# Optimization experiments

Measured on AMD Instinct MI355X. Metric: run time of the kernel, lower is better.

## Reference

```python
import jax, jax.numpy as jnp
import numpy as np

EPS = 1e-5          # nn.LayerNorm default eps
THRESH = 0.4        # min_entity_score
K = 20              # max_entities_per_text
NUM_TYPES = 8       # len(EntityType) (not in source; fixed constant)


def _mlp(x, w1, b1, g, be, w2, b2):
    """Linear -> LayerNorm -> GELU(exact) -> (Dropout=eval identity) -> Linear."""
    h = x @ w1 + b1
    mu = h.mean(-1, keepdims=True)
    var = ((h - mu) ** 2).mean(-1, keepdims=True)
    h = (h - mu) * jax.lax.rsqrt(var + EPS) * g + be
    h = jax.nn.gelu(h, approximate=False)
    return h @ w2 + b2


def setup_inputs() -> dict:
    key = jax.random.key(0)
    ks = jax.random.split(key, 10)
    B, S, D, H, T = 8, 4096, 1024, 256, NUM_TYPES

    def lin(k, i, o):
        s = 1.0 / np.sqrt(i)
        return jax.random.uniform(k, (i, o), jnp.float32, -s, s)

    return {
        "hidden_states": jax.random.normal(ks[0], (B, S, D), jnp.float32),
        "attention_mask": jax.random.randint(ks[1], (B, S), 0, 2).astype(jnp.int32),
        # entity_scorer params
        "sc_w1": lin(ks[2], D, H), "sc_b1": jnp.zeros((H,), jnp.float32),
        "sc_g": jnp.ones((H,), jnp.float32), "sc_be": jnp.zeros((H,), jnp.float32),
        "sc_w2": lin(ks[3], H, 1), "sc_b2": jnp.zeros((1,), jnp.float32),
        # span_enhancer params
        "en_w1": lin(ks[4], D, H), "en_b1": jnp.zeros((H,), jnp.float32),
        "en_g": jnp.ones((H,), jnp.float32), "en_be": jnp.zeros((H,), jnp.float32),
        "en_w2": lin(ks[5], H, D), "en_b2": jnp.zeros((D,), jnp.float32),
        # type_classifier params
        "ty_w1": lin(ks[6], D, H), "ty_b1": jnp.zeros((H,), jnp.float32),
        "ty_g": jnp.ones((H,), jnp.float32), "ty_be": jnp.zeros((H,), jnp.float32),
        "ty_w2": lin(ks[7], H, T), "ty_b2": jnp.zeros((T,), jnp.float32),
    }


def reference(hidden_states, attention_mask,
              sc_w1, sc_b1, sc_g, sc_be, sc_w2, sc_b2,
              en_w1, en_b1, en_g, en_be, en_w2, en_b2,
              ty_w1, ty_b1, ty_g, ty_be, ty_w2, ty_b2):
    B, S, D = hidden_states.shape
    # per-token entity scores [B, S]
    scores = jax.nn.sigmoid(_mlp(hidden_states, sc_w1, sc_b1, sc_g, sc_be, sc_w2, sc_b2))[..., 0]
    scores = scores * attention_mask.astype(scores.dtype)
    # parallel run-length encoding of spans (replaces serial python loop):
    # a token is inside a span iff score >= thresh and unmasked; spans break on
    # below-threshold or masked tokens, exactly as the serial RLE does.
    above = (scores >= THRESH) & (attention_mask > 0)
    prev = jnp.pad(above[:, :-1], ((0, 0), (1, 0)))
    start = above & ~prev
    sid = jnp.clip(jnp.cumsum(start.astype(jnp.int32), axis=1) - 1, 0)  # span label per token
    seg = (sid + jnp.arange(B, dtype=jnp.int32)[:, None] * S).reshape(-1)
    w = above.astype(scores.dtype)
    nseg = B * S
    span_len = jax.ops.segment_sum(w.reshape(-1), seg, num_segments=nseg).reshape(B, S)
    span_sum = jax.ops.segment_sum((scores * w).reshape(-1), seg, num_segments=nseg).reshape(B, S)
    rep_sum = jax.ops.segment_sum((hidden_states * w[..., None]).reshape(B * S, D), seg,
                                  num_segments=nseg).reshape(B, S, D)
    denom = jnp.maximum(span_len, 1.0)
    avg = span_sum / denom                      # mean token score per span
    valid = (span_len > 0) & (avg >= THRESH)    # avg-score threshold from original
    sel = jnp.where(valid, avg, -1.0)
    # keep at most K highest-scoring spans per batch row (matches global sort + per-batch cap)
    top_vals, top_idx = jax.lax.top_k(sel, K)   # [B, K]
    valid_k = (top_vals >= THRESH).astype(scores.dtype)
    reps = jnp.take_along_axis(rep_sum, top_idx[..., None], axis=1)
    lens = jnp.take_along_axis(denom, top_idx, axis=1)
    reps = reps / lens[..., None] * valid_k[..., None]      # span mean-pooled hidden states
    enhanced = _mlp(reps, en_w1, en_b1, en_g, en_be, en_w2, en_b2) * valid_k[..., None]
    type_logits = _mlp(enhanced, ty_w1, ty_b1, ty_g, ty_be, ty_w2, ty_b2)
    type_probs = jax.nn.softmax(type_logits, axis=-1)
    entity_types = jnp.argmax(type_logits, axis=-1)
    entity_scores = top_vals * valid_k
    return scores, enhanced, type_logits, entity_scores, type_probs, entity_types, valid_k
```

## Files before the change

kernel.cpp:

```cpp
#include <hip/hip_runtime.h>
#include <hip/hip_bf16.h>

#define S_LEN 4096
#define BATCH 8
#define DMODEL 1024
#define HDIM 256
#define NTYPES 8
#define KMAX 20
#define NSLOT (BATCH*KMAX)
#define THRESH 0.4f
#define LN_EPS 1e-5f
#define RSQRT2 0.70710678118654752f

#define O_SCORES 0
#define O_ENH    32768
#define O_TLOG   196608
#define O_ESC    197888
#define O_TPROB  198048
#define O_TYPE   199328
#define O_VALIDK 199488

#define WS_SCORES   0
#define WS_SPSTART  32768
#define WS_SPLEN    49152
#define WS_SPAVG    65536
#define WS_NSP      81920
#define WS_SELSTART 81936
#define WS_SELLEN   82096
#define WS_SELAVG   82256
#define WS_SELVALID 82416
#define WS_IMG      82576

typedef _Float16 f16x2 __attribute__((ext_vector_type(2)));
typedef _Float16 f16x8 __attribute__((ext_vector_type(8)));
typedef float f32x16 __attribute__((ext_vector_type(16)));

__device__ __forceinline__ float gelu_exact(float v) {
    return 0.5f * v * (1.0f + erff(v * RSQRT2));
}

__global__ __launch_bounds__(256) void k_prep(
    const float* __restrict__ W1, _Float16* __restrict__ IMG)
{
    const int c = blockIdx.x;
    const int n = threadIdx.x;
    f16x8 hv[2], lv[2];
#pragma unroll
    for (int j = 0; j < 2; j++)
#pragma unroll
        for (int e = 0; e < 8; e++) {
            float w = W1[(size_t)(c * 16 + j * 8 + e) * HDIM + n];
            _Float16 h = (_Float16)w;
            hv[j][e] = h;
            lv[j][e] = (_Float16)(w - (float)h);
        }
    const int off = c * 8192 + n * 16;
    *(f16x8*)&IMG[off] = hv[0];
    *(f16x8*)&IMG[off + 8] = hv[1];
    *(f16x8*)&IMG[off + 4096] = lv[0];
    *(f16x8*)&IMG[off + 4096 + 8] = lv[1];
}

__global__ __launch_bounds__(512, 4) void k_score6(
    const float* __restrict__ X, const _Float16* __restrict__ IMG,
    const float* __restrict__ B1, const float* __restrict__ G,
    const float* __restrict__ BE, const float* __restrict__ W2,
    const float* __restrict__ B2, const int* __restrict__ MASK,
    float* __restrict__ scf, float* __restrict__ out)
{
    union SM {
        _Float16 A[2][2][1024];
        struct { float part2[64 * 5]; float mul[64]; float rsl[64]; } e;
    };
    __shared__ SM sm;

    const int tid = threadIdx.x;
    const int lane = tid & 63, wid = tid >> 6;
    const int lr = lane & 31, lh = lane >> 5;
    const int wm = (wid & 1) * 32;
    const int wn = (wid >> 1) * 64;
    const int wnid = wid >> 1;
    const int tok0 = blockIdx.x * 64;

    const int xrow = tid >> 3, xk = (tid & 7) * 2;
    const float* xbase = X + (size_t)(tok0 + xrow) * DMODEL + xk;
    const int awoff = xrow * 16 + xk;
    const int aroff = (wm + lr) * 16 + lh * 8;
    const int bo0 = (wn + lr) * 16 + lh * 8;
    const int bo1 = (wn + 32 + lr) * 16 + lh * 8;

    f32x16 acc0 = (f32x16)0.0f, acc1 = (f32x16)0.0f;

    float2 x0 = *(const float2*)xbase;
    f16x8 bh0c = *(const f16x8*)&IMG[bo0];
    f16x8 bh1c = *(const f16x8*)&IMG[bo1];
    f16x8 bl0c = *(const f16x8*)&IMG[4096 + bo0];
    f16x8 bl1c = *(const f16x8*)&IMG[4096 + bo1];
    {
        _Float16 h0 = (_Float16)x0.x, h1 = (_Float16)x0.y;
        f16x2 hh = {h0, h1};
        f16x2 ll = {(_Float16)(x0.x - (float)h0), (_Float16)(x0.y - (float)h1)};
        *(f16x2*)&sm.A[0][0][awoff] = hh;
        *(f16x2*)&sm.A[0][1][awoff] = ll;
    }
    float2 xnext = *(const float2*)(xbase + 16);
    f16x8 bh0n = *(const f16x8*)&IMG[8192 + bo0];
    f16x8 bh1n = *(const f16x8*)&IMG[8192 + bo1];
    f16x8 bl0n = *(const f16x8*)&IMG[8192 + 4096 + bo0];
    f16x8 bl1n = *(const f16x8*)&IMG[8192 + 4096 + bo1];
    asm volatile("s_waitcnt lgkmcnt(0)" ::: "memory");
    __builtin_amdgcn_s_barrier();
    __builtin_amdgcn_sched_barrier(0);

    int cur = 0;
#pragma unroll 2
    for (int c = 0; c < 64; ++c) {
        const int cf = (c + 2) & 63;
        float2 xfut = *(const float2*)(xbase + cf * 16);
        const _Float16* ib = IMG + cf * 8192;
        f16x8 fbh0 = *(const f16x8*)&ib[bo0];
        f16x8 fbh1 = *(const f16x8*)&ib[bo1];
        f16x8 fbl0 = *(const f16x8*)&ib[4096 + bo0];
        f16x8 fbl1 = *(const f16x8*)&ib[4096 + bo1];

        f16x8 fah = *(const f16x8*)&sm.A[cur][0][aroff];
        f16x8 fal = *(const f16x8*)&sm.A[cur][1][aroff];

        acc0 = __builtin_amdgcn_mfma_f32_32x32x16_f16(fah, bh0c, acc0, 0, 0, 0);
        acc0 = __builtin_amdgcn_mfma_f32_32x32x16_f16(fal, bh0c, acc0, 0, 0, 0);
        acc0 = __builtin_amdgcn_mfma_f32_32x32x16_f16(fah, bl0c, acc0, 0, 0, 0);
        acc1 = __builtin_amdgcn_mfma_f32_32x32x16_f16(fah, bh1c, acc1, 0, 0, 0);
        acc1 = __builtin_amdgcn_mfma_f32_32x32x16_f16(fal, bh1c, acc1, 0, 0, 0);
        acc1 = __builtin_amdgcn_mfma_f32_32x32x16_f16(fah, bl1c, acc1, 0, 0, 0);

        {
            _Float16 h0 = (_Float16)xnext.x, h1 = (_Float16)xnext.y;
            f16x2 hh = {h0, h1};
            f16x2 ll = {(_Float16)(xnext.x - (float)h0), (_Float16)(xnext.y - (float)h1)};
            *(f16x2*)&sm.A[cur ^ 1][0][awoff] = hh;
            *(f16x2*)&sm.A[cur ^ 1][1][awoff] = ll;
        }
        asm volatile("s_waitcnt lgkmcnt(0)" ::: "memory");
        __builtin_amdgcn_s_barrier();
        __builtin_amdgcn_sched_barrier(0);

        bh0c = bh0n; bh1c = bh1n; bl0c = bl0n; bl1c = bl1n;
        bh0n = fbh0; bh1n = fbh1; bl0n = fbl0; bl1n = fbl1;
        xnext = xfut;
        cur ^= 1;
    }

    __syncthreads();

    float bcol[2], gcol[2], becol[2], wcol[2];
#pragma unroll
    for (int ni = 0; ni < 2; ni++) {
        int colg = wn + ni * 32 + lr;
        bcol[ni] = B1[colg];
        gcol[ni] = G[colg];
        becol[ni] = BE[colg];
        wcol[ni] = W2[colg];
    }
#pragma unroll
    for (int r = 0; r < 16; r++) { acc0[r] += bcol[0]; acc1[r] += bcol[1]; }

#pragma unroll
    for (int r = 0; r < 16; r++) {
        float p = acc0[r] + acc1[r];
        p += __shfl_xor(p, 1);  p += __shfl_xor(p, 2);
        p += __shfl_xor(p, 4);  p += __shfl_xor(p, 8);
        p += __shfl_xor(p, 16);
        int row = wm + (r & 3) + 8 * (r >> 2) + 4 * lh;
        if (lr == 0) sm.e.part2[row * 5 + wnid] = p;
    }
    __syncthreads();
    if (tid < 64)
        sm.e.mul[tid] = (sm.e.part2[tid * 5] + sm.e.part2[tid * 5 + 1] +
                         sm.e.part2[tid * 5 + 2] + sm.e.part2[tid * 5 + 3]) * (1.0f / 256.0f);
    __syncthreads();
#pragma unroll
    for (int r = 0; r < 16; r++) {
        int row = wm + (r & 3) + 8 * (r >> 2) + 4 * lh;
        float m = sm.e.mul[row];
        float d0 = acc0[r] - m, d1 = acc1[r] - m;
        float p = d0 * d0 + d1 * d1;
        p += __shfl_xor(p, 1);  p += __shfl_xor(p, 2);
        p += __shfl_xor(p, 4);  p += __shfl_xor(p, 8);
        p += __shfl_xor(p, 16);
        if (lr == 0) sm.e.part2[row * 5 + wnid] = p;
    }
    __syncthreads();
    if (tid < 64)
        sm.e.rsl[tid] = rsqrtf((sm.e.part2[tid * 5] + sm.e.part2[tid * 5 + 1] +
                                sm.e.part2[tid * 5 + 2] + sm.e.part2[tid * 5 + 3]) * (1.0f / 256.0f) + LN_EPS);
    __syncthreads();
#pragma unroll
    for (int r = 0; r < 16; r++) {
        int row = wm + (r & 3) + 8 * (r >> 2) + 4 * lh;
        float m = sm.e.mul[row];
        float rv = sm.e.rsl[row];
        float v0 = (acc0[r] - m) * rv * gcol[0] + becol[0];
        float v1 = (acc1[r] - m) * rv * gcol[1] + becol[1];
        float p = gelu_exact(v0) * wcol[0] + gelu_exact(v1) * wcol[1];
        p += __shfl_xor(p, 1);  p += __shfl_xor(p, 2);
        p += __shfl_xor(p, 4);  p += __shfl_xor(p, 8);
        p += __shfl_xor(p, 16);
        if (lr == 0) sm.e.part2[row * 5 + wnid] = p;
    }
    __syncthreads();
    if (tid < 64) {
        float s = sm.e.part2[tid * 5] + sm.e.part2[tid * 5 + 1] +
                  sm.e.part2[tid * 5 + 2] + sm.e.part2[tid * 5 + 3];
        float logit = s + B2[0];
        float sc = 1.0f / (1.0f + expf(-logit));
        int t = tok0 + tid;
        sc *= (float)MASK[t];
        scf[t] = sc;
        out[O_SCORES + t] = sc;
    }
}

__global__ __launch_bounds__(1024) void k_spans(
    const float* __restrict__ scf, int* __restrict__ spstart,
    int* __restrict__ splen, float* __restrict__ spavg, int* __restrict__ nsp,
    int* __restrict__ selstart, int* __restrict__ sellen,
    float* __restrict__ selavg, float* __restrict__ selvalid,
    float* __restrict__ out)
{
    const int r = blockIdx.x, tid = threadIdx.x;
    __shared__ float sc[S_LEN];
    __shared__ unsigned char ab[S_LEN];
    __shared__ int scn[1024];
    __shared__ float avgl[2048];
    __shared__ float rv[16];
    __shared__ int ri[16];

    float4 v = ((const float4*)(scf + (size_t)r * S_LEN))[tid];
    const int s0 = tid * 4;
    sc[s0 + 0] = v.x; sc[s0 + 1] = v.y; sc[s0 + 2] = v.z; sc[s0 + 3] = v.w;
    ab[s0 + 0] = (v.x >= THRESH);
    ab[s0 + 1] = (v.y >= THRESH);
    ab[s0 + 2] = (v.z >= THRESH);
    ab[s0 + 3] = (v.w >= THRESH);
    __syncthreads();

    bool st[4];
    int cnt = 0;
#pragma unroll
    for (int i = 0; i < 4; i++) {
        bool a = ab[s0 + i] != 0;
        bool p = (s0 + i == 0) ? false : (ab[s0 + i - 1] != 0);
        st[i] = a && !p;
        cnt += st[i] ? 1 : 0;
    }
    scn[tid] = cnt;
    __syncthreads();
    for (int off = 1; off < 1024; off <<= 1) {
        int mine = scn[tid];
        int add = (tid >= off) ? scn[tid - off] : 0;
        __syncthreads();
        scn[tid] = mine + add;
        __syncthreads();
    }
    const int total = scn[1023];
    int j = scn[tid] - cnt;
    for (int i = 0; i < 4; i++) {
        if (st[i]) {
            int s = s0 + i;
            float sum = 0.0f;
            int len = 0;
            int e = s;
            while (e < S_LEN && ab[e]) { sum += sc[e]; len++; e++; }
            float avg = sum / (float)len;
            spstart[r * 2048 + j] = s;
            splen[r * 2048 + j] = len;
            spavg[r * 2048 + j] = avg;
            avgl[j] = avg;
            j++;
        }
    }
    if (tid == 0) nsp[r] = total;
    __syncthreads();

    for (int k = 0; k < KMAX; k++) {
        float bv = -3.0e38f;
        int bi = 0x7FFFFFFF;
        for (int q = tid; q < total; q += 1024) {
            float a = avgl[q];
            if (a > bv) { bv = a; bi = q; }
        }
#pragma unroll
        for (int m = 1; m < 64; m <<= 1) {
            float ov = __shfl_xor(bv, m);
            int oi = __shfl_xor(bi, m);
            if (ov > bv || (ov == bv && oi < bi)) { bv = ov; bi = oi; }
        }
        if ((tid & 63) == 0) { rv[tid >> 6] = bv; ri[tid >> 6] = bi; }
        __syncthreads();
        if (tid < 64) {
            float v2 = (tid < 16) ? rv[tid] : -3.0e38f;
            int i2 = (tid < 16) ? ri[tid] : 0x7FFFFFFF;
#pragma unroll
            for (int m = 1; m < 16; m <<= 1) {
                float ov = __shfl_xor(v2, m);
                int oi = __shfl_xor(i2, m);
                if (ov > v2 || (ov == v2 && oi < i2)) { v2 = ov; i2 = oi; }
            }
            if (tid == 0) {
                int slot = r * KMAX + k;
                if (k < total) {
                    avgl[i2] = -3.0e38f;
                    int ln = splen[r * 2048 + i2];
                    float vd = (v2 >= THRESH && ln > 0) ? 1.0f : 0.0f;
                    selstart[slot] = spstart[r * 2048 + i2];
                    sellen[slot] = ln;
                    selavg[slot] = v2;
                    selvalid[slot] = vd;
                    out[O_ESC + slot] = v2 * vd;
                    out[O_VALIDK + slot] = vd;
                } else {
                    selstart[slot] = -1;
                    sellen[slot] = 0;
                    selavg[slot] = -1.0f;
                    selvalid[slot] = 0.0f;
                    out[O_ESC + slot] = 0.0f;
                    out[O_VALIDK + slot] = 0.0f;
                }
            }
        }
        __syncthreads();
    }
}

__global__ __launch_bounds__(1024) void k_tail2(
    const float* __restrict__ X, const int* __restrict__ selstart,
    const int* __restrict__ sellen, const float* __restrict__ selvalid,
    const float* __restrict__ en_w1, const float* __restrict__ en_b1,
    const float* __restrict__ en_g, const float* __restrict__ en_be,
    const float* __restrict__ en_w2, const float* __restrict__ en_b2,
    const float* __restrict__ ty_w1, const float* __restrict__ ty_b1,
    const float* __restrict__ ty_g, const float* __restrict__ ty_be,
    const float* __restrict__ ty_w2, const float* __restrict__ ty_b2,
    float* __restrict__ out)
{
    const int slot = blockIdx.x, tid = threadIdx.x;
    __shared__ float xr[DMODEL];
    __shared__ float ps[DMODEL];
    __shared__ float g1[HDIM];
    __shared__ float red[8];
    __shared__ float lgp[4 * NTYPES];
    __shared__ float lg[NTYPES];

    const int r = slot / KMAX;
    const int s0 = selstart[slot], ln = sellen[slot];
    const float vd = selvalid[slot];
    const int j = tid & 255, p = tid >> 8;

    {
        float a = 0.0f;
        if (s0 >= 0) {
            const float* base = X + ((size_t)r * S_LEN + s0) * DMODEL + tid;
#pragma unroll 4
            for (int t = 0; t < ln; t++) a += base[(size_t)t * DMODEL];
        }
        const float dn = (ln > 0) ? (float)ln : 1.0f;
        xr[tid] = a / dn * vd;
    }
    __syncthreads();

    {
        float acc = 0.0f;
        const float* wp = en_w1 + (size_t)(p * 256) * HDIM + j;
        const float* xp = xr + p * 256;
#pragma unroll 16
        for (int k = 0; k < 256; k++) acc += xp[k] * wp[(size_t)k * HDIM];
        ps[tid] = acc;
    }
    __syncthreads();
    float h = 0.0f, mu = 0.0f;
    if (tid < 256) {
        h = ps[tid] + ps[256 + tid] + ps[512 + tid] + ps[768 + tid] + en_b1[tid];
        float s = h;
#pragma unroll
        for (int m = 1; m < 64; m <<= 1) s += __shfl_xor(s, m);
        if ((tid & 63) == 0) red[tid >> 6] = s;
    }
    __syncthreads();
    if (tid < 256) {
        mu = (red[0] + red[1] + red[2] + red[3]) * (1.0f / 256.0f);
        float d = h - mu;
        float s = d * d;
#pragma unroll
        for (int m = 1; m < 64; m <<= 1) s += __shfl_xor(s, m);
        if ((tid & 63) == 0) red[4 + (tid >> 6)] = s;
    }
    __syncthreads();
    if (tid < 256) {
        float var = (red[4] + red[5] + red[6] + red[7]) * (1.0f / 256.0f);
        float v = (h - mu) * rsqrtf(var + LN_EPS) * en_g[tid] + en_be[tid];
        g1[tid] = gelu_exact(v);
    }
    __syncthreads();

    {
        float acc = en_b2[tid];
        const float* wp = en_w2 + tid;
#pragma unroll 16
        for (int k = 0; k < 256; k++) acc += g1[k] * wp[(size_t)k * DMODEL];
        acc *= vd;
        out[O_ENH + (size_t)slot * DMODEL + tid] = acc;
        xr[tid] = acc;
    }
    __syncthreads();

    {
        float acc = 0.0f;
        const float* wp = ty_w1 + (size_t)(p * 256) * HDIM + j;
        const float* xp = xr + p * 256;
#pragma unroll 16
        for (int k = 0; k < 256; k++) acc += xp[k] * wp[(size_t)k * HDIM];
        ps[tid] = acc;
    }
    __syncthreads();
    h = 0.0f; mu = 0.0f;
    if (tid < 256) {
        h = ps[tid] + ps[256 + tid] + ps[512 + tid] + ps[768 + tid] + ty_b1[tid];
        float s = h;
#pragma unroll
        for (int m = 1; m < 64; m <<= 1) s += __shfl_xor(s, m);
        if ((tid & 63) == 0) red[tid >> 6] = s;
    }
    __syncthreads();
    if (tid < 256) {
        mu = (red[0] + red[1] + red[2] + red[3]) * (1.0f / 256.0f);
        float d = h - mu;
        float s = d * d;
#pragma unroll
        for (int m = 1; m < 64; m <<= 1) s += __shfl_xor(s, m);
        if ((tid & 63) == 0) red[4 + (tid >> 6)] = s;
    }
    __syncthreads();
    if (tid < 256) {
        float var = (red[4] + red[5] + red[6] + red[7]) * (1.0f / 256.0f);
        float v = (h - mu) * rsqrtf(var + LN_EPS) * ty_g[tid] + ty_be[tid];
        g1[tid] = gelu_exact(v);
    }
    __syncthreads();

    if (tid < 256) {
        float gv = g1[tid];
        float4 w0 = *(const float4*)&ty_w2[tid * NTYPES];
        float4 w1v = *(const float4*)&ty_w2[tid * NTYPES + 4];
        float pj[8] = {gv * w0.x, gv * w0.y, gv * w0.z, gv * w0.w,
                       gv * w1v.x, gv * w1v.y, gv * w1v.z, gv * w1v.w};
#pragma unroll
        for (int q = 0; q < 8; q++) {
            float s = pj[q];
#pragma unroll
            for (int m = 1; m < 64; m <<= 1) s += __shfl_xor(s, m);
            pj[q] = s;
        }
        if ((tid & 63) == 0) {
#pragma unroll
            for (int q = 0; q < 8; q++) lgp[(tid >> 6) * NTYPES + q] = pj[q];
        }
    }
    __syncthreads();
    if (tid < NTYPES) {
        float la = ty_b2[tid] + lgp[tid] + lgp[NTYPES + tid] +
                   lgp[2 * NTYPES + tid] + lgp[3 * NTYPES + tid];
        lg[tid] = la;
        out[O_TLOG + slot * NTYPES + tid] = la;
    }
    __syncthreads();
    if (tid == 0) {
        float mx = lg[0];
        int am = 0;
        for (int t = 1; t < NTYPES; t++)
            if (lg[t] > mx) { mx = lg[t]; am = t; }
        float ex[NTYPES], ssum = 0.0f;
        for (int t = 0; t < NTYPES; t++) { ex[t] = expf(lg[t] - mx); ssum += ex[t]; }
        for (int t = 0; t < NTYPES; t++)
            out[O_TPROB + slot * NTYPES + t] = ex[t] / ssum;
        out[O_TYPE + slot] = (float)am;
    }
}

extern "C" void kernel_launch(void* const* d_in, const int* in_sizes, int n_in,
                              void* d_out, int out_size, void* d_ws, size_t ws_size,
                              hipStream_t stream) {
    const float* X = (const float*)d_in[0];
    const int* MASK = (const int*)d_in[1];
    const float* sc_w1 = (const float*)d_in[2];
    const float* sc_b1 = (const float*)d_in[3];
    const float* sc_g  = (const float*)d_in[4];
    const float* sc_be = (const float*)d_in[5];
    const float* sc_w2 = (const float*)d_in[6];
    const float* sc_b2 = (const float*)d_in[7];
    const float* en_w1 = (const float*)d_in[8];
    const float* en_b1 = (const float*)d_in[9];
    const float* en_g  = (const float*)d_in[10];
    const float* en_be = (const float*)d_in[11];
    const float* en_w2 = (const float*)d_in[12];
    const float* en_b2 = (const float*)d_in[13];
    const float* ty_w1 = (const float*)d_in[14];
    const float* ty_b1 = (const float*)d_in[15];
    const float* ty_g  = (const float*)d_in[16];
    const float* ty_be = (const float*)d_in[17];
    const float* ty_w2 = (const float*)d_in[18];
    const float* ty_b2 = (const float*)d_in[19];

    float* out = (float*)d_out;
    float* wsf = (float*)d_ws;
    int* wsi = (int*)d_ws;
    _Float16* img = (_Float16*)(wsf + WS_IMG);

    k_prep<<<64, 256, 0, stream>>>(sc_w1, img);
    k_score6<<<(BATCH * S_LEN) / 64, 512, 0, stream>>>(
        X, img, sc_b1, sc_g, sc_be, sc_w2, sc_b2, MASK, wsf + WS_SCORES, out);
    k_spans<<<BATCH, 1024, 0, stream>>>(
        wsf + WS_SCORES, wsi + WS_SPSTART, wsi + WS_SPLEN, wsf + WS_SPAVG,
        wsi + WS_NSP, wsi + WS_SELSTART, wsi + WS_SELLEN, wsf + WS_SELAVG,
        wsf + WS_SELVALID, out);
    k_tail2<<<NSLOT, 1024, 0, stream>>>(
        X, wsi + WS_SELSTART, wsi + WS_SELLEN, wsf + WS_SELVALID,
        en_w1, en_b1, en_g, en_be, en_w2, en_b2,
        ty_w1, ty_b1, ty_g, ty_be, ty_w2, ty_b2, out);
}
```

Before: 164.1 us.

## Restructure score GEMM: 64-wide K stages, per-wave 32-column N split

Rewrites the scorer GEMM main loop. It stages 64 K-elements of X per barrier, padded in shared memory to stride 72, instead of 16, which cuts barriers from 64 to 32. Each wave now covers all 64 rows and a 32-column slice, so it loads one B fragment per K step and reuses it across two A fragments. This drops the explicit register double-buffering and prefetch pipeline, so weight loads are no longer prefetched ahead of the MFMAs and latency may be exposed. The LayerNorm reductions now combine 8 partials per row instead of 4.

After: 175.6 us. 1.07x slower.

```diff
diff --git a/kernel.cpp b/kernel.cpp
--- a/kernel.cpp
+++ b/kernel.cpp
@@ -31,9 +31,10 @@
 #define WS_SELVALID 82416
 #define WS_IMG      82576
 
-typedef _Float16 f16x2 __attribute__((ext_vector_type(2)));
 typedef _Float16 f16x8 __attribute__((ext_vector_type(8)));
 typedef float f32x16 __attribute__((ext_vector_type(16)));
+
+#define ARS 72
 
 __device__ __forceinline__ float gelu_exact(float v) {
     return 0.5f * v * (1.0f + erff(v * RSQRT2));
@@ -61,7 +62,7 @@
     *(f16x8*)&IMG[off + 4096 + 8] = lv[1];
 }
 
-__global__ __launch_bounds__(512, 4) void k_score6(
+__global__ __launch_bounds__(512, 4) void k_score8(
     const float* __restrict__ X, const _Float16* __restrict__ IMG,
     const float* __restrict__ B1, const float* __restrict__ G,
     const float* __restrict__ BE, const float* __restrict__ W2,
@@ -69,148 +70,148 @@
     float* __restrict__ scf, float* __restrict__ out)
 {
     union SM {
-        _Float16 A[2][2][1024];
-        struct { float part2[64 * 5]; float mul[64]; float rsl[64]; } e;
+        _Float16 A[2][64 * ARS];
+        struct { float part2[64 * 9]; float mul[64]; float rsl[64]; } e;
     };
     __shared__ SM sm;
 
     const int tid = threadIdx.x;
     const int lane = tid & 63, wid = tid >> 6;
     const int lr = lane & 31, lh = lane >> 5;
-    const int wm = (wid & 1) * 32;
-    const int wn = (wid >> 1) * 64;
-    const int wnid = wid >> 1;
+    const int wn = wid * 32;
     const int tok0 = blockIdx.x * 64;
 
-    const int xrow = tid >> 3, xk = (tid & 7) * 2;
-    const float* xbase = X + (size_t)(tok0 + xrow) * DMODEL + xk;
-    const int awoff = xrow * 16 + xk;
-    const int aroff = (wm + lr) * 16 + lh * 8;
-    const int bo0 = (wn + lr) * 16 + lh * 8;
-    const int bo1 = (wn + 32 + lr) * 16 + lh * 8;
+    const int xrow = tid >> 3, xkg = tid & 7;
+    const float* xbase = X + (size_t)(tok0 + xrow) * DMODEL + xkg * 8;
+    const int awoff = xrow * ARS + xkg * 8;
+    const int ar0 = lr * ARS + lh * 8;
+    const int ar1 = (32 + lr) * ARS + lh * 8;
+    const int bo = (wn + lr) * 16 + lh * 8;
 
     f32x16 acc0 = (f32x16)0.0f, acc1 = (f32x16)0.0f;
 
-    float2 x0 = *(const float2*)xbase;
-    f16x8 bh0c = *(const f16x8*)&IMG[bo0];
-    f16x8 bh1c = *(const f16x8*)&IMG[bo1];
-    f16x8 bl0c = *(const f16x8*)&IMG[4096 + bo0];
-    f16x8 bl1c = *(const f16x8*)&IMG[4096 + bo1];
-    {
-        _Float16 h0 = (_Float16)x0.x, h1 = (_Float16)x0.y;
-        f16x2 hh = {h0, h1};
-        f16x2 ll = {(_Float16)(x0.x - (float)h0), (_Float16)(x0.y - (float)h1)};
-        *(f16x2*)&sm.A[0][0][awoff] = hh;
-        *(f16x2*)&sm.A[0][1][awoff] = ll;
-    }
-    float2 xnext = *(const float2*)(xbase + 16);
-    f16x8 bh0n = *(const f16x8*)&IMG[8192 + bo0];
-    f16x8 bh1n = *(const f16x8*)&IMG[8192 + bo1];
-    f16x8 bl0n = *(const f16x8*)&IMG[8192 + 4096 + bo0];
-    f16x8 bl1n = *(const f16x8*)&IMG[8192 + 4096 + bo1];
-    asm volatile("s_waitcnt lgkmcnt(0)" ::: "memory");
-    __builtin_amdgcn_s_barrier();
-    __builtin_amdgcn_sched_barrier(0);
-
-    int cur = 0;
-#pragma unroll 2
-    for (int c = 0; c < 64; ++c) {
-        const int cf = (c + 2) & 63;
-        float2 xfut = *(const float2*)(xbase + cf * 16);
-        const _Float16* ib = IMG + cf * 8192;
-        f16x8 fbh0 = *(const f16x8*)&ib[bo0];
-        f16x8 fbh1 = *(const f16x8*)&ib[bo1];
-        f16x8 fbl0 = *(const f16x8*)&ib[4096 + bo0];
-        f16x8 fbl1 = *(const f16x8*)&ib[4096 + bo1];
-
-        f16x8 fah = *(const f16x8*)&sm.A[cur][0][aroff];
-        f16x8 fal = *(const f16x8*)&sm.A[cur][1][aroff];
-
-        acc0 = __builtin_amdgcn_mfma_f32_32x32x16_f16(fah, bh0c, acc0, 0, 0, 0);
-        acc0 = __builtin_amdgcn_mfma_f32_32x32x16_f16(fal, bh0c, acc0, 0, 0, 0);
-        acc0 = __builtin_amdgcn_mfma_f32_32x32x16_f16(fah, bl0c, acc0, 0, 0, 0);
-        acc1 = __builtin_amdgcn_mfma_f32_32x32x16_f16(fah, bh1c, acc1, 0, 0, 0);
-        acc1 = __builtin_amdgcn_mfma_f32_32x32x16_f16(fal, bh1c, acc1, 0, 0, 0);
-        acc1 = __builtin_amdgcn_mfma_f32_32x32x16_f16(fah, bl1c, acc1, 0, 0, 0);
-
+    float4 xa = *(const float4*)xbase;
+    float4 xb = *(const float4*)(xbase + 4);
+
+    for (int s = 0; s < 16; ++s) {
         {
-            _Float16 h0 = (_Float16)xnext.x, h1 = (_Float16)xnext.y;
-            f16x2 hh = {h0, h1};
-            f16x2 ll = {(_Float16)(xnext.x - (float)h0), (_Float16)(xnext.y - (float)h1)};
-            *(f16x2*)&sm.A[cur ^ 1][0][awoff] = hh;
-            *(f16x2*)&sm.A[cur ^ 1][1][awoff] = ll;
-        }
-        asm volatile("s_waitcnt lgkmcnt(0)" ::: "memory");
-        __builtin_amdgcn_s_barrier();
-        __builtin_amdgcn_sched_barrier(0);
-
-        bh0c = bh0n; bh1c = bh1n; bl0c = bl0n; bl1c = bl1n;
-        bh0n = fbh0; bh1n = fbh1; bl0n = fbl0; bl1n = fbl1;
-        xnext = xfut;
-        cur ^= 1;
-    }
-
-    __syncthreads();
-
-    float bcol[2], gcol[2], becol[2], wcol[2];
-#pragma unroll
-    for (int ni = 0; ni < 2; ni++) {
-        int colg = wn + ni * 32 + lr;
-        bcol[ni] = B1[colg];
-        gcol[ni] = G[colg];
-        becol[ni] = BE[colg];
-        wcol[ni] = W2[colg];
-    }
-#pragma unroll
-    for (int r = 0; r < 16; r++) { acc0[r] += bcol[0]; acc1[r] += bcol[1]; }
+            float xv[8] = {xa.x, xa.y, xa.z, xa.w, xb.x, xb.y, xb.z, xb.w};
+            f16x8 ah, al;
+#pragma unroll
+            for (int e = 0; e < 8; e++) {
+                _Float16 h = (_Float16)xv[e];
+                ah[e] = h;
+                al[e] = (_Float16)(xv[e] - (float)h);
+            }
+            *(f16x8*)&sm.A[0][awoff] = ah;
+            *(f16x8*)&sm.A[1][awoff] = al;
+        }
+        __syncthreads();
+
+        if (s < 15) {
+            xa = *(const float4*)(xbase + (s + 1) * 64);
+            xb = *(const float4*)(xbase + (s + 1) * 64 + 4);
+        }
+
+#pragma unroll
+        for (int kk = 0; kk < 4; ++kk) {
+            const _Float16* ib = IMG + (size_t)(s * 4 + kk) * 8192;
+            f16x8 bh = *(const f16x8*)&ib[bo];
+            f16x8 bl = *(const f16x8*)&ib[4096 + bo];
+            f16x8 fa0h = *(const f16x8*)&sm.A[0][ar0 + kk * 16];
+            f16x8 fa0l = *(const f16x8*)&sm.A[1][ar0 + kk * 16];
+            f16x8 fa1h = *(const f16x8*)&sm.A[0][ar1 + kk * 16];
+            f16x8 fa1l = *(const f16x8*)&sm.A[1][ar1 + kk * 16];
+            acc0 = __builtin_amdgcn_mfma_f32_32x32x16_f16(fa0h, bh, acc0, 0, 0, 0);
+            acc0 = __builtin_amdgcn_mfma_f32_32x32x16_f16(fa0l, bh, acc0, 0, 0, 0);
+            acc0 = __builtin_amdgcn_mfma_f32_32x32x16_f16(fa0h, bl, acc0, 0, 0, 0);
+            acc1 = __builtin_amdgcn_mfma_f32_32x32x16_f16(fa1h, bh, acc1, 0, 0, 0);
+            acc1 = __builtin_amdgcn_mfma_f32_32x32x16_f16(fa1l, bh, acc1, 0, 0, 0);
+            acc1 = __builtin_amdgcn_mfma_f32_32x32x16_f16(fa1h, bl, acc1, 0, 0, 0);
+        }
+        __syncthreads();
+    }
+
+    const float bc = B1[wn + lr];
+    const float gc = G[wn + lr];
+    const float bec = BE[wn + lr];
+    const float wc = W2[wn + lr];
+#pragma unroll
+    for (int r = 0; r < 16; r++) { acc0[r] += bc; acc1[r] += bc; }
 
 #pragma unroll
     for (int r = 0; r < 16; r++) {
-        float p = acc0[r] + acc1[r];
-        p += __shfl_xor(p, 1);  p += __shfl_xor(p, 2);
-        p += __shfl_xor(p, 4);  p += __shfl_xor(p, 8);
-        p += __shfl_xor(p, 16);
-        int row = wm + (r & 3) + 8 * (r >> 2) + 4 * lh;
-        if (lr == 0) sm.e.part2[row * 5 + wnid] = p;
-    }
-    __syncthreads();
-    if (tid < 64)
-        sm.e.mul[tid] = (sm.e.part2[tid * 5] + sm.e.part2[tid * 5 + 1] +
-                         sm.e.part2[tid * 5 + 2] + sm.e.part2[tid * 5 + 3]) * (1.0f / 256.0f);
+        float p0 = acc0[r], p1 = acc1[r];
+        p0 += __shfl_xor(p0, 1);  p0 += __shfl_xor(p0, 2);
+        p0 += __shfl_xor(p0, 4);  p0 += __shfl_xor(p0, 8);
+        p0 += __shfl_xor(p0, 16);
+        p1 += __shfl_xor(p1, 1);  p1 += __shfl_xor(p1, 2);
+        p1 += __shfl_xor(p1, 4);  p1 += __shfl_xor(p1, 8);
+        p1 += __shfl_xor(p1, 16);
+        int row = (r & 3) + 8 * (r >> 2) + 4 * lh;
+        if (lr == 0) {
+            sm.e.part2[row * 9 + wid] = p0;
+            sm.e.part2[(row + 32) * 9 + wid] = p1;
+        }
+    }
+    __syncthreads();
+    if (tid < 64) {
+        float s = 0.0f;
+#pragma unroll
+        for (int w = 0; w < 8; w++) s += sm.e.part2[tid * 9 + w];
+        sm.e.mul[tid] = s * (1.0f / 256.0f);
+    }
     __syncthreads();
 #pragma unroll
     for (int r = 0; r < 16; r++) {
-        int row = wm + (r & 3) + 8 * (r >> 2) + 4 * lh;
-        float m = sm.e.mul[row];
-        float d0 = acc0[r] - m, d1 = acc1[r] - m;
-        float p = d0 * d0 + d1 * d1;
-        p += __shfl_xor(p, 1);  p += __shfl_xor(p, 2);
-        p += __shfl_xor(p, 4);  p += __shfl_xor(p, 8);
-        p += __shfl_xor(p, 16);
-        if (lr == 0) sm.e.part2[row * 5 + wnid] = p;
-    }
-    __syncthreads();
-    if (tid < 64)
-        sm.e.rsl[tid] = rsqrtf((sm.e.part2[tid * 5] + sm.e.part2[tid * 5 + 1] +
-                                sm.e.part2[tid * 5 + 2] + sm.e.part2[tid * 5 + 3]) * (1.0f / 256.0f) + LN_EPS);
+        int row = (r & 3) + 8 * (r >> 2) + 4 * lh;
+        float m0 = sm.e.mul[row], m1 = sm.e.mul[row + 32];
+        float d0 = acc0[r] - m0, d1 = acc1[r] - m1;
+        float p0 = d0 * d0, p1 = d1 * d1;
+        p0 += __shfl_xor(p0, 1);  p0 += __shfl_xor(p0, 2);
+        p0 += __shfl_xor(p0, 4);  p0 += __shfl_xor(p0, 8);
+        p0 += __shfl_xor(p0, 16);
+        p1 += __shfl_xor(p1, 1);  p1 += __shfl_xor(p1, 2);
+        p1 += __shfl_xor(p1, 4);  p1 += __shfl_xor(p1, 8);
+        p1 += __shfl_xor(p1, 16);
+        if (lr == 0) {
+            sm.e.part2[row * 9 + wid] = p0;
+            sm.e.part2[(row + 32) * 9 + wid] = p1;
+        }
+    }
+    __syncthreads();
+    if (tid < 64) {
+        float s = 0.0f;
+#pragma unroll
+        for (int w = 0; w < 8; w++) s += sm.e.part2[tid * 9 + w];
+        sm.e.rsl[tid] = rsqrtf(s * (1.0f / 256.0f) + LN_EPS);
+    }
     __syncthreads();
 #pragma unroll
     for (int r = 0; r < 16; r++) {
-        int row = wm + (r & 3) + 8 * (r >> 2) + 4 * lh;
-        float m = sm.e.mul[row];
-        float rv = sm.e.rsl[row];
-        float v0 = (acc0[r] - m) * rv * gcol[0] + becol[0];
-        float v1 = (acc1[r] - m) * rv * gcol[1] + becol[1];
-        float p = gelu_exact(v0) * wcol[0] + gelu_exact(v1) * wcol[1];
-        p += __shfl_xor(p, 1);  p += __shfl_xor(p, 2);
-        p += __shfl_xor(p, 4);  p += __shfl_xor(p, 8);
-        p += __shfl_xor(p, 16);
-        if (lr == 0) sm.e.part2[row * 5 + wnid] = p;
+        int row = (r & 3) + 8 * (r >> 2) + 4 * lh;
+        float m0 = sm.e.mul[row], m1 = sm.e.mul[row + 32];
+        float rv0 = sm.e.rsl[row], rv1 = sm.e.rsl[row + 32];
+        float v0 = (acc0[r] - m0) * rv0 * gc + bec;
+        float v1 = (acc1[r] - m1) * rv1 * gc + bec;
+        float p0 = gelu_exact(v0) * wc;
+        float p1 = gelu_exact(v1) * wc;
+        p0 += __shfl_xor(p0, 1);  p0 += __shfl_xor(p0, 2);
+        p0 += __shfl_xor(p0, 4);  p0 += __shfl_xor(p0, 8);
+        p0 += __shfl_xor(p0, 16);
+        p1 += __shfl_xor(p1, 1);  p1 += __shfl_xor(p1, 2);
+        p1 += __shfl_xor(p1, 4);  p1 += __shfl_xor(p1, 8);
+        p1 += __shfl_xor(p1, 16);
+        if (lr == 0) {
+            sm.e.part2[row * 9 + wid] = p0;
+            sm.e.part2[(row + 32) * 9 + wid] = p1;
+        }
     }
     __syncthreads();
     if (tid < 64) {
-        float s = sm.e.part2[tid * 5] + sm.e.part2[tid * 5 + 1] +
-                  sm.e.part2[tid * 5 + 2] + sm.e.part2[tid * 5 + 3];
+        float s = 0.0f;
+#pragma unroll
+        for (int w = 0; w < 8; w++) s += sm.e.part2[tid * 9 + w];
         float logit = s + B2[0];
         float sc = 1.0f / (1.0f + expf(-logit));
         int t = tok0 + tid;
@@ -516,7 +517,7 @@
     _Float16* img = (_Float16*)(wsf + WS_IMG);
 
     k_prep<<<64, 256, 0, stream>>>(sc_w1, img);
-    k_score6<<<(BATCH * S_LEN) / 64, 512, 0, stream>>>(
+    k_score8<<<(BATCH * S_LEN) / 64, 512, 0, stream>>>(
         X, img, sc_b1, sc_g, sc_be, sc_w2, sc_b2, MASK, wsf + WS_SCORES, out);
     k_spans<<<BATCH, 1024, 0, stream>>>(
         wsf + WS_SCORES, wsi + WS_SPSTART, wsi + WS_SPLEN, wsf + WS_SPAVG,
```
